# Kernel tuning notes

Hardware: AMD Instinct MI355X
Metric: run time of the kernel (lower is better)

## Reference

```python
import jax, jax.numpy as jnp
import numpy as np

B, NG, H, G, T0, T1 = 4096, 3000, 6, 30, 500, 50  # batch, genes, hidden, genes/term, leaf terms, mid terms
EPS = 1e-5  # BatchNorm1d default eps


def _bn(x, gamma, beta):
    # training-mode BatchNorm1d: biased batch stats over the batch axis
    m = x.mean(axis=0)
    v = ((x - m) ** 2).mean(axis=0)
    return gamma * (x - m) / jnp.sqrt(v + EPS) + beta


def setup_inputs() -> dict:
    key = jax.random.key(0)
    ks = iter(jax.random.split(key, 32))
    rn = lambda shape, s=0.05: jax.random.normal(next(ks), shape, dtype=jnp.float32) * s
    return dict(
        cell_features=jax.random.normal(next(ks), (B, NG), dtype=jnp.float32),
        Wdg=rn((T0 + T1 + 1, G, NG)), bdg=rn((T0 + T1 + 1, G)),
        W0=rn((T0, H, G)), b0=rn((T0, H)), gam0=jnp.ones((T0, H), jnp.float32), bet0=jnp.zeros((T0, H), jnp.float32),
        aw0=rn((T0, H)), ab0=rn((T0,)), av0=rn((T0,)), ac0=rn((T0,)),
        W1=rn((T1, H, 10 * H + G)), b1=rn((T1, H)), gam1=jnp.ones((T1, H), jnp.float32), bet1=jnp.zeros((T1, H), jnp.float32),
        aw1=rn((T1, H)), ab1=rn((T1,)), av1=rn((T1,)), ac1=rn((T1,)),
        W2=rn((H, T1 * H + G)), b2=rn((H,)), gam2=jnp.ones((H,), jnp.float32), bet2=jnp.zeros((H,), jnp.float32),
        aw2=rn((H,)), ab2=rn(()), av2=rn(()), ac2=rn(()),
    )


def reference(cell_features, Wdg, bdg,
              W0, b0, gam0, bet0, aw0, ab0, av0, ac0,
              W1, b1, gam1, bet1, aw1, ab1, av1, ac1,
              W2, b2, gam2, bet2, aw2, ab2, av2, ac2):
    # direct_gene_layer for every term: Linear(ngene -> genes_per_term), no activation
    dg = jnp.einsum('bn,tgn->btg', cell_features, Wdg) + bdg  # [B, 551, G]
    # ---- layer 0 (leaves): input = direct gene output only ----
    z0 = jnp.tanh(jnp.einsum('btg,thg->bth', dg[:, :T0], W0) + b0)
    n0 = _bn(z0, gam0, bet0)                                   # [B, T0, H]
    aux0 = jnp.tanh(jnp.einsum('bth,th->bt', n0, aw0) + ab0) * av0 + ac0
    # ---- layer 1: term t's children are leaves [10t, 10t+10); concat children + direct genes ----
    in1 = jnp.concatenate([n0.reshape(B, T1, 10 * H), dg[:, T0:T0 + T1]], axis=-1)  # [B, T1, 90]
    z1 = jnp.tanh(jnp.einsum('bti,thi->bth', in1, W1) + b1)
    n1 = _bn(z1, gam1, bet1)                                   # [B, T1, H]
    aux1 = jnp.tanh(jnp.einsum('bth,th->bt', n1, aw1) + ab1) * av1 + ac1
    # ---- root: children = all mid terms + direct genes ----
    in2 = jnp.concatenate([n1.reshape(B, T1 * H), dg[:, -1]], axis=-1)  # [B, 330]
    z2 = jnp.tanh(in2 @ W2.T + b2)
    n2 = _bn(z2, gam2, bet2)                                   # [B, H]
    aux2 = jnp.tanh(n2 @ aw2 + ab2) * av2 + ac2                # [B]
    # flatten (aux_out_map, term_NN_out_map) into one array for a single comparable output
    aux_all = jnp.concatenate([aux0, aux1, aux2[:, None]], axis=1)              # [B, 551]
    nn_all = jnp.concatenate([n0.reshape(B, -1), n1.reshape(B, -1), n2], axis=1)  # [B, 551*H]
    return jnp.concatenate([aux_all, nn_all], axis=1)          # [B, 3857]
```

## Files before the change

### kernel.cpp

```cpp
#include <hip/hip_runtime.h>
#include <hip/hip_bf16.h>

#define BATCH 4096
#define NGENE 3000
#define HID   6
#define GPT   30
#define T0N   500
#define T1N   50
#define KP    3008
#define MROWS 4608
#define OUTW  3857
#define BNEPS 1e-5f
#define NKT   47
#define BUFU  16384

typedef __attribute__((ext_vector_type(8))) __bf16 bf16x8;
typedef __attribute__((ext_vector_type(4))) float f32x4;
typedef __attribute__((ext_vector_type(8))) unsigned short ushort8;

__device__ __forceinline__ unsigned short f2bf(float f) {
  unsigned int u = __builtin_bit_cast(unsigned int, f);
  u = (u + 0x7fffu + ((u >> 16) & 1u)) >> 16;
  return (unsigned short)u;
}

__device__ __forceinline__ void gload_lds16(const void* g, void* l) {
  __builtin_amdgcn_global_load_lds(
      (const __attribute__((address_space(1))) unsigned int*)g,
      (__attribute__((address_space(3))) unsigned int*)l, 16, 0, 0);
}

__global__ void prep(const float* __restrict__ cell, const float* __restrict__ Wdg,
                     const float* __restrict__ bdg, const float* __restrict__ W0,
                     const float* __restrict__ b0,
                     ushort8* __restrict__ cellb, ushort8* __restrict__ abuf8,
                     float* __restrict__ bias) {
  int blk = blockIdx.x;
  if (blk < 6016) {
    int idx = blk * 256 + threadIdx.x;
    int r = idx / 376, c8 = idx - r * 376;
    int c = c8 * 8;
    ushort8 o = (ushort8)0;
    if (c < NGENE) {
      const float4* p = (const float4*)(cell + (size_t)r * NGENE + c);
      float4 a = p[0], b = p[1];
      o[0] = f2bf(a.x); o[1] = f2bf(a.y); o[2] = f2bf(a.z); o[3] = f2bf(a.w);
      o[4] = f2bf(b.x); o[5] = f2bf(b.y); o[6] = f2bf(b.z); o[7] = f2bf(b.w);
    }
    cellb[idx] = o;
  } else if (blk < 8378) {
    int idx = (blk - 6016) * 256 + threadIdx.x;
    if (idx >= 1608 * 376) return;
    int r = idx / 376, c8 = idx - r * 376;
    int c = c8 * 8;
    ushort8 o = (ushort8)0;
    if (r < 1530 && c < NGENE) {
      const float4* p = (const float4*)(Wdg + (size_t)(15000 + r) * NGENE + c);
      float4 a = p[0], b = p[1];
      o[0] = f2bf(a.x); o[1] = f2bf(a.y); o[2] = f2bf(a.z); o[3] = f2bf(a.w);
      o[4] = f2bf(b.x); o[5] = f2bf(b.y); o[6] = f2bf(b.z); o[7] = f2bf(b.w);
    }
    abuf8[(size_t)(3000 + r) * 376 + c8] = o;
  } else {
    int idx = (blk - 8378) * 256 + threadIdx.x;
    if (idx >= MROWS) return;
    float v = 0.f;
    if (idx < 3000) {
      int t = idx / HID;
      float s = b0[idx];
#pragma unroll
      for (int g = 0; g < GPT; ++g) s += W0[idx * GPT + g] * bdg[t * GPT + g];
      v = s;
    } else if (idx < 4530) {
      v = bdg[15000 + idx - 3000];
    }
    bias[idx] = v;
  }
}

__global__ void v0_build(const float* __restrict__ Wdg, const float* __restrict__ W0,
                         unsigned short* __restrict__ abuf) {
  int n = blockIdx.x * 256 + threadIdx.x;
  int t = blockIdx.y;
  if (n >= KP) return;
  bool valid = n < NGENE;
  float x[GPT];
#pragma unroll
  for (int g = 0; g < GPT; ++g)
    x[g] = valid ? Wdg[((size_t)(t * GPT + g)) * NGENE + n] : 0.f;
#pragma unroll
  for (int h = 0; h < HID; ++h) {
    const float* w = W0 + (t * HID + h) * GPT;
    float s = 0.f;
#pragma unroll
    for (int g = 0; g < GPT; ++g) s += x[g] * w[g];
    abuf[((size_t)(t * HID + h)) * KP + n] = valid ? f2bf(s) : (unsigned short)0;
  }
}

__global__ __launch_bounds__(256, 2) void gemm_fused(
    const unsigned short* __restrict__ A,
    const unsigned short* __restrict__ Bt,
    const float* __restrict__ bias,
    float* __restrict__ C,
    float* __restrict__ st) {
  extern __shared__ unsigned short smem[];
  const int tid  = threadIdx.x;
  const int wave = tid >> 6, lane = tid & 63;
  const int wm = wave >> 1, wn = wave & 1;
  const int quad = lane >> 4, fr = lane & 15;

  const int bid = blockIdx.x;
  const int wg  = (bid & 7) * 144 + (bid >> 3);
  const int m0 = (wg >> 5) * 128;
  const int n0 = (wg & 31) * 128;

  const unsigned short* srcA[4];
  const unsigned short* srcB[4];
#pragma unroll
  for (int i = 0; i < 4; ++i) {
    int c = i * 256 + tid;
    int row = c >> 3, sl = c & 7;
    srcA[i] = A  + (size_t)(m0 + row) * KP + ((sl ^ (row & 7)) << 3);
    srcB[i] = Bt + (size_t)(n0 + row) * KP + ((sl ^ (row & 7)) << 3);
  }

  f32x4 acc[4][4] = {};

#define STAGE(kt, buf)                                                        \
  {                                                                           \
    unsigned short* bb = smem + (buf) * BUFU;                                 \
    const int ko = (kt) * 64;                                                 \
    _Pragma("unroll")                                                         \
    for (int i = 0; i < 4; ++i) {                                             \
      gload_lds16(srcA[i] + ko, bb + i * 2048 + wave * 512);                  \
      gload_lds16(srcB[i] + ko, bb + 8192 + i * 2048 + wave * 512);           \
    }                                                                         \
  }

  STAGE(0, 0);
  STAGE(1, 1);
  asm volatile("s_waitcnt vmcnt(8)" ::: "memory");
  __builtin_amdgcn_s_barrier();

  const int ks0 = (quad ^ (fr & 7)) << 3;
  const int arow = (wm * 64 + fr) * 64;
  const int brow = 8192 + (wn * 64 + fr) * 64;

  int cur = 0;
  for (int t = 0; t < NKT; ++t) {
    const unsigned short* Ab = smem + cur * BUFU;
    bf16x8 af[4][2], bf[4][2];
#pragma unroll
    for (int tm = 0; tm < 4; ++tm) {
      af[tm][0] = *(const bf16x8*)(Ab + arow + tm * 1024 + ks0);
      af[tm][1] = *(const bf16x8*)(Ab + arow + tm * 1024 + (ks0 ^ 32));
    }
#pragma unroll
    for (int tn = 0; tn < 4; ++tn) {
      bf[tn][0] = *(const bf16x8*)(Ab + brow + tn * 1024 + ks0);
      bf[tn][1] = *(const bf16x8*)(Ab + brow + tn * 1024 + (ks0 ^ 32));
    }
    asm volatile("s_waitcnt lgkmcnt(0)" ::: "memory");
    __builtin_amdgcn_s_barrier();
    if (t + 2 < NKT) STAGE(t + 2, cur);
    __builtin_amdgcn_s_setprio(1);
#pragma unroll
    for (int s = 0; s < 2; ++s)
#pragma unroll
      for (int i = 0; i < 4; ++i)
#pragma unroll
        for (int j = 0; j < 4; ++j)
          acc[i][j] = __builtin_amdgcn_mfma_f32_16x16x32_bf16(af[i][s], bf[j][s], acc[i][j], 0, 0, 0);
    __builtin_amdgcn_s_setprio(0);
    if (t + 2 < NKT)      asm volatile("s_waitcnt vmcnt(8)" ::: "memory");
    else if (t + 1 < NKT) asm volatile("s_waitcnt vmcnt(0)" ::: "memory");
    __builtin_amdgcn_s_barrier();
    cur ^= 1;
  }
#undef STAGE

  const int mbase = m0 + wm * 64 + quad * 4;
  const int nbase = n0 + wn * 64 + fr;
#pragma unroll
  for (int i = 0; i < 4; ++i) {
#pragma unroll
    for (int rr = 0; rr < 4; ++rr) {
      const int m = mbase + i * 16 + rr;
      const float bia = bias[m];
      const bool act = m < 3000;
      float s = 0.f, q = 0.f;
#pragma unroll
      for (int j = 0; j < 4; ++j) {
        float v = acc[i][j][rr] + bia;
        if (act) v = tanhf(v);
        C[(size_t)m * BATCH + nbase + j * 16] = v;
        s += v; q += v * v;
      }
      if (act) {
#pragma unroll
        for (int off = 1; off < 16; off <<= 1) {
          s += __shfl_xor(s, off);
          q += __shfl_xor(q, off);
        }
        if (fr == 0) {
          atomicAdd(&st[2 * m], s);
          atomicAdd(&st[2 * m + 1], q);
        }
      }
    }
  }
}

__global__ void bnfin(const float* __restrict__ st, const float* __restrict__ gam,
                      const float* __restrict__ bet, float* __restrict__ ss, int ncols) {
  int c = blockIdx.x * 256 + threadIdx.x;
  if (c >= ncols) return;
  float m = st[2 * c] * (1.f / BATCH);
  float v = st[2 * c + 1] * (1.f / BATCH) - m * m;
  float sc = gam[c] * rsqrtf(v + BNEPS);
  ss[2 * c] = sc;
  ss[2 * c + 1] = bet[c] - m * sc;
}

__global__ void norm_emit_aux(const float* __restrict__ zT, const float* __restrict__ ss,
                              const float* __restrict__ aw, const float* __restrict__ ab,
                              const float* __restrict__ av, const float* __restrict__ ac,
                              float* __restrict__ out, int ncols, int outoff,
                              int auxoff, int nterm) {
  __shared__ float tile[66][65];
  int lane = threadIdx.x & 63, w = threadIdx.x >> 6;
  int c0 = blockIdx.x * 66, b0 = blockIdx.y * 64;
  for (int cc = w; cc < 66; cc += 4) {
    int c = c0 + cc;
    float n = 0.f;
    if (c < ncols)
      n = zT[(size_t)c * BATCH + b0 + lane] * ss[2 * c] + ss[2 * c + 1];
    tile[cc][lane] = n;
  }
  __syncthreads();
  for (int cl = lane; cl < 66; cl += 64) {
    int c = c0 + cl;
    if (c < ncols) {
#pragma unroll
      for (int i = 0; i < 16; ++i) {
        int rr = w * 16 + i;
        out[(size_t)(b0 + rr) * OUTW + outoff + c] = tile[cl][rr];
      }
    }
  }
  int t0 = c0 / 6;
  for (int tl = w; tl < 11; tl += 4) {
    int t = t0 + tl;
    if (t < nterm && c0 + tl * 6 < ncols) {
      float s = ab[t];
#pragma unroll
      for (int h = 0; h < HID; ++h) s += tile[tl * 6 + h][lane] * aw[t * HID + h];
      out[(size_t)(b0 + lane) * OUTW + auxoff + t] = tanhf(s) * av[t] + ac[t];
    }
  }
}

__global__ void layer1_zT(const float* __restrict__ C, const float* __restrict__ ss0,
                          const float* __restrict__ W1, const float* __restrict__ b1,
                          float* __restrict__ z1T, float* __restrict__ st) {
  int lane = threadIdx.x & 63, tg = threadIdx.x >> 6;
  int t = blockIdx.x * 4 + tg;
  if (t >= T1N) return;
  int b = blockIdx.y * 64 + lane;
  const float* z0T = C;
  const float* dgm = C + (size_t)3000 * BATCH;
  float x[90];
#pragma unroll
  for (int j = 0; j < 60; ++j) {
    int c = t * 60 + j;
    x[j] = z0T[(size_t)c * BATCH + b] * ss0[2 * c] + ss0[2 * c + 1];
  }
#pragma unroll
  for (int g = 0; g < GPT; ++g)
    x[60 + g] = dgm[(size_t)(t * GPT + g) * BATCH + b];
#pragma unroll
  for (int h = 0; h < HID; ++h) {
    int c = t * HID + h;
    const float* w = W1 + c * 90;
    float s = b1[c];
#pragma unroll
    for (int i = 0; i < 90; ++i) s += x[i] * w[i];
    float z = tanhf(s);
    z1T[(size_t)c * BATCH + b] = z;
    float s1 = z, s2 = z * z;
#pragma unroll
    for (int off = 32; off > 0; off >>= 1) {
      s1 += __shfl_down(s1, off);
      s2 += __shfl_down(s2, off);
    }
    if (lane == 0) {
      atomicAdd(&st[2 * c], s1);
      atomicAdd(&st[2 * c + 1], s2);
    }
  }
}

__global__ void root_zT(const float* __restrict__ C, const float* __restrict__ z1T,
                        const float* __restrict__ ss1, const float* __restrict__ W2,
                        const float* __restrict__ b2, float* __restrict__ z2T,
                        float* __restrict__ st) {
  int b = blockIdx.x * 256 + threadIdx.x;
  int lane = threadIdx.x & 63;
  const float* dgr = C + (size_t)4500 * BATCH;
  float s[HID];
#pragma unroll
  for (int h = 0; h < HID; ++h) s[h] = b2[h];
  for (int c = 0; c < 300; ++c) {
    float n = z1T[(size_t)c * BATCH + b] * ss1[2 * c] + ss1[2 * c + 1];
#pragma unroll
    for (int h = 0; h < HID; ++h) s[h] += n * W2[h * 330 + c];
  }
#pragma unroll
  for (int g = 0; g < GPT; ++g) {
    float d = dgr[(size_t)g * BATCH + b];
#pragma unroll
    for (int h = 0; h < HID; ++h) s[h] += d * W2[h * 330 + 300 + g];
  }
#pragma unroll
  for (int h = 0; h < HID; ++h) {
    float z = tanhf(s[h]);
    z2T[(size_t)h * BATCH + b] = z;
    float s1 = z, s2 = z * z;
#pragma unroll
    for (int off = 32; off > 0; off >>= 1) {
      s1 += __shfl_down(s1, off);
      s2 += __shfl_down(s2, off);
    }
    if (lane == 0) {
      atomicAdd(&st[2 * h], s1);
      atomicAdd(&st[2 * h + 1], s2);
    }
  }
}

__global__ void root_emit(const float* __restrict__ z2T, const float* __restrict__ ss2,
                          const float* __restrict__ aw2, const float* __restrict__ ab2,
                          const float* __restrict__ av2, const float* __restrict__ ac2,
                          float* __restrict__ out) {
  int b = blockIdx.x * 256 + threadIdx.x;
  float s = ab2[0];
#pragma unroll
  for (int h = 0; h < HID; ++h) {
    float n = z2T[(size_t)h * BATCH + b] * ss2[2 * h] + ss2[2 * h + 1];
    out[(size_t)b * OUTW + 3851 + h] = n;
    s += n * aw2[h];
  }
  out[(size_t)b * OUTW + 550] = tanhf(s) * av2[0] + ac2[0];
}

extern "C" void kernel_launch(void* const* d_in, const int* in_sizes, int n_in,
                              void* d_out, int out_size, void* d_ws, size_t ws_size,
                              hipStream_t stream) {
  (void)in_sizes; (void)n_in; (void)out_size; (void)ws_size;
  const float* cell = (const float*)d_in[0];
  const float* Wdg  = (const float*)d_in[1];
  const float* bdg  = (const float*)d_in[2];
  const float* W0   = (const float*)d_in[3];
  const float* b0   = (const float*)d_in[4];
  const float* gam0 = (const float*)d_in[5];
  const float* bet0 = (const float*)d_in[6];
  const float* aw0  = (const float*)d_in[7];
  const float* ab0  = (const float*)d_in[8];
  const float* av0  = (const float*)d_in[9];
  const float* ac0  = (const float*)d_in[10];
  const float* W1   = (const float*)d_in[11];
  const float* b1   = (const float*)d_in[12];
  const float* gam1 = (const float*)d_in[13];
  const float* bet1 = (const float*)d_in[14];
  const float* aw1  = (const float*)d_in[15];
  const float* ab1  = (const float*)d_in[16];
  const float* av1  = (const float*)d_in[17];
  const float* ac1  = (const float*)d_in[18];
  const float* W2   = (const float*)d_in[19];
  const float* b2   = (const float*)d_in[20];
  const float* gam2 = (const float*)d_in[21];
  const float* bet2 = (const float*)d_in[22];
  const float* aw2  = (const float*)d_in[23];
  const float* ab2  = (const float*)d_in[24];
  const float* av2  = (const float*)d_in[25];
  const float* ac2  = (const float*)d_in[26];
  float* out = (float*)d_out;

  char* ws = (char*)d_ws;
  unsigned short* cellb = (unsigned short*)(ws);
  unsigned short* abuf  = (unsigned short*)(ws + 24641536);
  float*          C     = (float*)(ws + 52363264);
  float*          z1T   = (float*)(ws + 127860736);
  float*          z2T   = (float*)(ws + 132775936);
  float*          st    = (float*)(ws + 132874240);
  float*          ssb   = (float*)(ws + 132907008);
  float*          bias  = (float*)(ws + 132939776);
  float* st0 = st,  *st1 = st + 2 * 3000,  *st2 = st + 2 * 3300;
  float* ss0 = ssb, *ss1 = ssb + 2 * 3000, *ss2 = ssb + 2 * 3300;

  static int s_attr = 0;
  if (!s_attr) {
    hipFuncSetAttribute(reinterpret_cast<const void*>(gemm_fused),
                        hipFuncAttributeMaxDynamicSharedMemorySize, 65536);
    s_attr = 1;
  }

  hipMemsetAsync(st, 0, 32768, stream);
  prep<<<8396, 256, 0, stream>>>(cell, Wdg, bdg, W0, b0,
                                 (ushort8*)cellb, (ushort8*)abuf, bias);
  v0_build<<<dim3(12, T0N), 256, 0, stream>>>(Wdg, W0, abuf);

  gemm_fused<<<1152, 256, 65536, stream>>>(abuf, cellb, bias, C, st0);

  bnfin<<<12, 256, 0, stream>>>(st0, gam0, bet0, ss0, 3000);
  norm_emit_aux<<<dim3(46, 64), 256, 0, stream>>>(C, ss0, aw0, ab0, av0, ac0,
                                                  out, 3000, 551, 0, 500);

  layer1_zT<<<dim3(13, 64), 256, 0, stream>>>(C, ss0, W1, b1, z1T, st1);
  bnfin<<<2, 256, 0, stream>>>(st1, gam1, bet1, ss1, 300);
  norm_emit_aux<<<dim3(5, 64), 256, 0, stream>>>(z1T, ss1, aw1, ab1, av1, ac1,
                                                 out, 300, 3551, 500, 50);

  root_zT<<<16, 256, 0, stream>>>(C, z1T, ss1, W2, b2, z2T, st2);
  bnfin<<<1, 256, 0, stream>>>(st2, gam2, bet2, ss2, 6);
  root_emit<<<16, 256, 0, stream>>>(z2T, ss2, aw2, ab2, av2, ac2, out);
}
```

Before: 699.9 us.

## Fuse BN-finalize and post-GEMM layers into fewer kernels, split MFMA halves

The separate bnfin launches are folded into their consumers, which now compute scale and shift from the raw sums. Layer-0 normalize/emit/aux is merged with the layer-1 compute, and layer-1 emit is merged with the root compute in one launch. This cuts kernel launches and avoids re-reading C for the normalized layer-0 values. The GEMM drops its XCD-aware block swizzle for a plain 2D grid, and issues the first half of the MFMAs before the LDS barrier to overlap LDS reads with compute. The root path still runs in only 16 blocks inside fuse_l2, and the plain grid may lose L2 locality.

```diff
diff --git a/kernel.cpp b/kernel.cpp
--- a/kernel.cpp
+++ b/kernel.cpp
@@ -110,10 +110,8 @@
   const int wm = wave >> 1, wn = wave & 1;
   const int quad = lane >> 4, fr = lane & 15;
 
-  const int bid = blockIdx.x;
-  const int wg  = (bid & 7) * 144 + (bid >> 3);
-  const int m0 = (wg >> 5) * 128;
-  const int n0 = (wg & 31) * 128;
+  const int m0 = blockIdx.y * 128;
+  const int n0 = blockIdx.x * 128;
 
   const unsigned short* srcA[4];
   const unsigned short* srcB[4];
@@ -152,26 +150,29 @@
     const unsigned short* Ab = smem + cur * BUFU;
     bf16x8 af[4][2], bf[4][2];
 #pragma unroll
-    for (int tm = 0; tm < 4; ++tm) {
-      af[tm][0] = *(const bf16x8*)(Ab + arow + tm * 1024 + ks0);
-      af[tm][1] = *(const bf16x8*)(Ab + arow + tm * 1024 + (ks0 ^ 32));
-    }
-#pragma unroll
-    for (int tn = 0; tn < 4; ++tn) {
-      bf[tn][0] = *(const bf16x8*)(Ab + brow + tn * 1024 + ks0);
-      bf[tn][1] = *(const bf16x8*)(Ab + brow + tn * 1024 + (ks0 ^ 32));
-    }
+    for (int tm = 0; tm < 4; ++tm) af[tm][0] = *(const bf16x8*)(Ab + arow + tm * 1024 + ks0);
+#pragma unroll
+    for (int tn = 0; tn < 4; ++tn) bf[tn][0] = *(const bf16x8*)(Ab + brow + tn * 1024 + ks0);
+#pragma unroll
+    for (int tm = 0; tm < 4; ++tm) af[tm][1] = *(const bf16x8*)(Ab + arow + tm * 1024 + (ks0 ^ 32));
+#pragma unroll
+    for (int tn = 0; tn < 4; ++tn) bf[tn][1] = *(const bf16x8*)(Ab + brow + tn * 1024 + (ks0 ^ 32));
+    __builtin_amdgcn_s_setprio(1);
+#pragma unroll
+    for (int i = 0; i < 4; ++i)
+#pragma unroll
+      for (int j = 0; j < 4; ++j)
+        acc[i][j] = __builtin_amdgcn_mfma_f32_16x16x32_bf16(af[i][0], bf[j][0], acc[i][j], 0, 0, 0);
+    __builtin_amdgcn_s_setprio(0);
     asm volatile("s_waitcnt lgkmcnt(0)" ::: "memory");
     __builtin_amdgcn_s_barrier();
     if (t + 2 < NKT) STAGE(t + 2, cur);
     __builtin_amdgcn_s_setprio(1);
 #pragma unroll
-    for (int s = 0; s < 2; ++s)
-#pragma unroll
-      for (int i = 0; i < 4; ++i)
-#pragma unroll
-        for (int j = 0; j < 4; ++j)
-          acc[i][j] = __builtin_amdgcn_mfma_f32_16x16x32_bf16(af[i][s], bf[j][s], acc[i][j], 0, 0, 0);
+    for (int i = 0; i < 4; ++i)
+#pragma unroll
+      for (int j = 0; j < 4; ++j)
+        acc[i][j] = __builtin_amdgcn_mfma_f32_16x16x32_bf16(af[i][1], bf[j][1], acc[i][j], 0, 0, 0);
     __builtin_amdgcn_s_setprio(0);
     if (t + 2 < NKT)      asm volatile("s_waitcnt vmcnt(8)" ::: "memory");
     else if (t + 1 < NKT) asm volatile("s_waitcnt vmcnt(0)" ::: "memory");
@@ -212,134 +213,155 @@
   }
 }
 
-__global__ void bnfin(const float* __restrict__ st, const float* __restrict__ gam,
-                      const float* __restrict__ bet, float* __restrict__ ss, int ncols) {
-  int c = blockIdx.x * 256 + threadIdx.x;
-  if (c >= ncols) return;
-  float m = st[2 * c] * (1.f / BATCH);
-  float v = st[2 * c + 1] * (1.f / BATCH) - m * m;
-  float sc = gam[c] * rsqrtf(v + BNEPS);
-  ss[2 * c] = sc;
-  ss[2 * c + 1] = bet[c] - m * sc;
-}
-
-__global__ void norm_emit_aux(const float* __restrict__ zT, const float* __restrict__ ss,
-                              const float* __restrict__ aw, const float* __restrict__ ab,
-                              const float* __restrict__ av, const float* __restrict__ ac,
-                              float* __restrict__ out, int ncols, int outoff,
-                              int auxoff, int nterm) {
-  __shared__ float tile[66][65];
-  int lane = threadIdx.x & 63, w = threadIdx.x >> 6;
-  int c0 = blockIdx.x * 66, b0 = blockIdx.y * 64;
-  for (int cc = w; cc < 66; cc += 4) {
-    int c = c0 + cc;
-    float n = 0.f;
-    if (c < ncols)
-      n = zT[(size_t)c * BATCH + b0 + lane] * ss[2 * c] + ss[2 * c + 1];
-    tile[cc][lane] = n;
+__global__ void fuse_l1(const float* __restrict__ C, const float* __restrict__ st0,
+                        const float* __restrict__ gam0, const float* __restrict__ bet0,
+                        const float* __restrict__ aw0, const float* __restrict__ ab0,
+                        const float* __restrict__ av0, const float* __restrict__ ac0,
+                        const float* __restrict__ W1, const float* __restrict__ b1,
+                        float* __restrict__ out, float* __restrict__ z1T,
+                        float* __restrict__ st1) {
+  __shared__ float tile[60][65];
+  __shared__ float dgt[30][65];
+  __shared__ float ssl[120];
+  const int t = blockIdx.x, b0 = blockIdx.y * 64;
+  const int lane = threadIdx.x & 63, w = threadIdx.x >> 6;
+  if (threadIdx.x < 60) {
+    int c = t * 60 + threadIdx.x;
+    float m = st0[2 * c] * (1.f / BATCH);
+    float v = st0[2 * c + 1] * (1.f / BATCH) - m * m;
+    float sc = gam0[c] * rsqrtf(v + BNEPS);
+    ssl[2 * threadIdx.x] = sc;
+    ssl[2 * threadIdx.x + 1] = bet0[c] - m * sc;
   }
   __syncthreads();
-  for (int cl = lane; cl < 66; cl += 64) {
-    int c = c0 + cl;
-    if (c < ncols) {
-#pragma unroll
-      for (int i = 0; i < 16; ++i) {
-        int rr = w * 16 + i;
-        out[(size_t)(b0 + rr) * OUTW + outoff + c] = tile[cl][rr];
-      }
-    }
-  }
-  int t0 = c0 / 6;
-  for (int tl = w; tl < 11; tl += 4) {
-    int t = t0 + tl;
-    if (t < nterm && c0 + tl * 6 < ncols) {
-      float s = ab[t];
-#pragma unroll
-      for (int h = 0; h < HID; ++h) s += tile[tl * 6 + h][lane] * aw[t * HID + h];
-      out[(size_t)(b0 + lane) * OUTW + auxoff + t] = tanhf(s) * av[t] + ac[t];
-    }
-  }
-}
-
-__global__ void layer1_zT(const float* __restrict__ C, const float* __restrict__ ss0,
-                          const float* __restrict__ W1, const float* __restrict__ b1,
-                          float* __restrict__ z1T, float* __restrict__ st) {
-  int lane = threadIdx.x & 63, tg = threadIdx.x >> 6;
-  int t = blockIdx.x * 4 + tg;
-  if (t >= T1N) return;
-  int b = blockIdx.y * 64 + lane;
-  const float* z0T = C;
-  const float* dgm = C + (size_t)3000 * BATCH;
-  float x[90];
-#pragma unroll
-  for (int j = 0; j < 60; ++j) {
-    int c = t * 60 + j;
-    x[j] = z0T[(size_t)c * BATCH + b] * ss0[2 * c] + ss0[2 * c + 1];
-  }
-#pragma unroll
-  for (int g = 0; g < GPT; ++g)
-    x[60 + g] = dgm[(size_t)(t * GPT + g) * BATCH + b];
-#pragma unroll
-  for (int h = 0; h < HID; ++h) {
-    int c = t * HID + h;
-    const float* w = W1 + c * 90;
-    float s = b1[c];
-#pragma unroll
-    for (int i = 0; i < 90; ++i) s += x[i] * w[i];
-    float z = tanhf(s);
-    z1T[(size_t)c * BATCH + b] = z;
-    float s1 = z, s2 = z * z;
-#pragma unroll
-    for (int off = 32; off > 0; off >>= 1) {
-      s1 += __shfl_down(s1, off);
-      s2 += __shfl_down(s2, off);
-    }
-    if (lane == 0) {
-      atomicAdd(&st[2 * c], s1);
-      atomicAdd(&st[2 * c + 1], s2);
-    }
-  }
-}
-
-__global__ void root_zT(const float* __restrict__ C, const float* __restrict__ z1T,
-                        const float* __restrict__ ss1, const float* __restrict__ W2,
-                        const float* __restrict__ b2, float* __restrict__ z2T,
-                        float* __restrict__ st) {
-  int b = blockIdx.x * 256 + threadIdx.x;
-  int lane = threadIdx.x & 63;
-  const float* dgr = C + (size_t)4500 * BATCH;
-  float s[HID];
-#pragma unroll
-  for (int h = 0; h < HID; ++h) s[h] = b2[h];
-  for (int c = 0; c < 300; ++c) {
-    float n = z1T[(size_t)c * BATCH + b] * ss1[2 * c] + ss1[2 * c + 1];
-#pragma unroll
-    for (int h = 0; h < HID; ++h) s[h] += n * W2[h * 330 + c];
-  }
-#pragma unroll
-  for (int g = 0; g < GPT; ++g) {
-    float d = dgr[(size_t)g * BATCH + b];
-#pragma unroll
-    for (int h = 0; h < HID; ++h) s[h] += d * W2[h * 330 + 300 + g];
-  }
-#pragma unroll
-  for (int h = 0; h < HID; ++h) {
-    float z = tanhf(s[h]);
-    z2T[(size_t)h * BATCH + b] = z;
-    float s1 = z, s2 = z * z;
-#pragma unroll
-    for (int off = 32; off > 0; off >>= 1) {
-      s1 += __shfl_down(s1, off);
-      s2 += __shfl_down(s2, off);
-    }
-    if (lane == 0) {
-      atomicAdd(&st[2 * h], s1);
-      atomicAdd(&st[2 * h + 1], s2);
-    }
-  }
-}
-
-__global__ void root_emit(const float* __restrict__ z2T, const float* __restrict__ ss2,
+  for (int cc = w; cc < 60; cc += 4)
+    tile[cc][lane] = C[(size_t)(t * 60 + cc) * BATCH + b0 + lane] * ssl[2 * cc] + ssl[2 * cc + 1];
+  for (int g = w; g < GPT; g += 4)
+    dgt[g][lane] = C[(size_t)(3000 + t * GPT + g) * BATCH + b0 + lane];
+  __syncthreads();
+  if (lane < 60) {
+#pragma unroll
+    for (int i = 0; i < 16; ++i)
+      out[(size_t)(b0 + w * 16 + i) * OUTW + 551 + t * 60 + lane] = tile[lane][w * 16 + i];
+  }
+  for (int tl = w; tl < 10; tl += 4) {
+    int tt = t * 10 + tl;
+    float s = ab0[tt];
+#pragma unroll
+    for (int h = 0; h < HID; ++h) s += tile[tl * 6 + h][lane] * aw0[tt * HID + h];
+    out[(size_t)(b0 + lane) * OUTW + tt] = tanhf(s) * av0[tt] + ac0[tt];
+  }
+  if (w < 3) {
+#pragma unroll
+    for (int hh = 0; hh < 2; ++hh) {
+      int h = w * 2 + hh, c = t * HID + h;
+      const float* wr = W1 + c * 90;
+      float s = b1[c];
+#pragma unroll
+      for (int j = 0; j < 60; ++j) s += tile[j][lane] * wr[j];
+#pragma unroll
+      for (int g = 0; g < GPT; ++g) s += dgt[g][lane] * wr[60 + g];
+      float z = tanhf(s);
+      z1T[(size_t)c * BATCH + b0 + lane] = z;
+      float s1 = z, s2 = z * z;
+#pragma unroll
+      for (int off = 32; off > 0; off >>= 1) {
+        s1 += __shfl_down(s1, off);
+        s2 += __shfl_down(s2, off);
+      }
+      if (lane == 0) {
+        atomicAdd(&st1[2 * c], s1);
+        atomicAdd(&st1[2 * c + 1], s2);
+      }
+    }
+  }
+}
+
+__global__ void fuse_l2(const float* __restrict__ C, const float* __restrict__ z1T,
+                        const float* __restrict__ st1,
+                        const float* __restrict__ gam1, const float* __restrict__ bet1,
+                        const float* __restrict__ aw1, const float* __restrict__ ab1,
+                        const float* __restrict__ av1, const float* __restrict__ ac1,
+                        const float* __restrict__ W2, const float* __restrict__ b2,
+                        float* __restrict__ out, float* __restrict__ z2T,
+                        float* __restrict__ st2) {
+  const int blk = blockIdx.x;
+  if (blk < 320) {
+    __shared__ float tile[60][65];
+    __shared__ float ssl[120];
+    const int q = blk >> 6, b0 = (blk & 63) * 64;
+    const int lane = threadIdx.x & 63, w = threadIdx.x >> 6;
+    if (threadIdx.x < 60) {
+      int c = q * 60 + threadIdx.x;
+      float m = st1[2 * c] * (1.f / BATCH);
+      float v = st1[2 * c + 1] * (1.f / BATCH) - m * m;
+      float sc = gam1[c] * rsqrtf(v + BNEPS);
+      ssl[2 * threadIdx.x] = sc;
+      ssl[2 * threadIdx.x + 1] = bet1[c] - m * sc;
+    }
+    __syncthreads();
+    for (int cc = w; cc < 60; cc += 4)
+      tile[cc][lane] = z1T[(size_t)(q * 60 + cc) * BATCH + b0 + lane] * ssl[2 * cc] + ssl[2 * cc + 1];
+    __syncthreads();
+    if (lane < 60) {
+#pragma unroll
+      for (int i = 0; i < 16; ++i)
+        out[(size_t)(b0 + w * 16 + i) * OUTW + 3551 + q * 60 + lane] = tile[lane][w * 16 + i];
+    }
+    for (int tl = w; tl < 10; tl += 4) {
+      int tt = q * 10 + tl;
+      float s = ab1[tt];
+#pragma unroll
+      for (int h = 0; h < HID; ++h) s += tile[tl * 6 + h][lane] * aw1[tt * HID + h];
+      out[(size_t)(b0 + lane) * OUTW + 500 + tt] = tanhf(s) * av1[tt] + ac1[tt];
+    }
+  } else {
+    __shared__ float ssl[600];
+    const int b = (blk - 320) * 256 + threadIdx.x;
+    const int lane = threadIdx.x & 63;
+    for (int c = threadIdx.x; c < 300; c += 256) {
+      float m = st1[2 * c] * (1.f / BATCH);
+      float v = st1[2 * c + 1] * (1.f / BATCH) - m * m;
+      float sc = gam1[c] * rsqrtf(v + BNEPS);
+      ssl[2 * c] = sc;
+      ssl[2 * c + 1] = bet1[c] - m * sc;
+    }
+    __syncthreads();
+    const float* dgr = C + (size_t)4500 * BATCH;
+    float s[HID];
+#pragma unroll
+    for (int h = 0; h < HID; ++h) s[h] = b2[h];
+    for (int c = 0; c < 300; ++c) {
+      float n = z1T[(size_t)c * BATCH + b] * ssl[2 * c] + ssl[2 * c + 1];
+#pragma unroll
+      for (int h = 0; h < HID; ++h) s[h] += n * W2[h * 330 + c];
+    }
+#pragma unroll
+    for (int g = 0; g < GPT; ++g) {
+      float d = dgr[(size_t)g * BATCH + b];
+#pragma unroll
+      for (int h = 0; h < HID; ++h) s[h] += d * W2[h * 330 + 300 + g];
+    }
+#pragma unroll
+    for (int h = 0; h < HID; ++h) {
+      float z = tanhf(s[h]);
+      z2T[(size_t)h * BATCH + b] = z;
+      float s1 = z, s2 = z * z;
+#pragma unroll
+      for (int off = 32; off > 0; off >>= 1) {
+        s1 += __shfl_down(s1, off);
+        s2 += __shfl_down(s2, off);
+      }
+      if (lane == 0) {
+        atomicAdd(&st2[2 * h], s1);
+        atomicAdd(&st2[2 * h + 1], s2);
+      }
+    }
+  }
+}
+
+__global__ void root_emit(const float* __restrict__ z2T, const float* __restrict__ st2,
+                          const float* __restrict__ gam2, const float* __restrict__ bet2,
                           const float* __restrict__ aw2, const float* __restrict__ ab2,
                           const float* __restrict__ av2, const float* __restrict__ ac2,
                           float* __restrict__ out) {
@@ -347,7 +369,11 @@
   float s = ab2[0];
 #pragma unroll
   for (int h = 0; h < HID; ++h) {
-    float n = z2T[(size_t)h * BATCH + b] * ss2[2 * h] + ss2[2 * h + 1];
+    float m = st2[2 * h] * (1.f / BATCH);
+    float v = st2[2 * h + 1] * (1.f / BATCH) - m * m;
+    float sc = gam2[h] * rsqrtf(v + BNEPS);
+    float sh = bet2[h] - m * sc;
+    float n = z2T[(size_t)h * BATCH + b] * sc + sh;
     out[(size_t)b * OUTW + 3851 + h] = n;
     s += n * aw2[h];
   }
@@ -394,10 +420,8 @@
   float*          z1T   = (float*)(ws + 127860736);
   float*          z2T   = (float*)(ws + 132775936);
   float*          st    = (float*)(ws + 132874240);
-  float*          ssb   = (float*)(ws + 132907008);
   float*          bias  = (float*)(ws + 132939776);
-  float* st0 = st,  *st1 = st + 2 * 3000,  *st2 = st + 2 * 3300;
-  float* ss0 = ssb, *ss1 = ssb + 2 * 3000, *ss2 = ssb + 2 * 3300;
+  float* st0 = st, *st1 = st + 2 * 3000, *st2 = st + 2 * 3300;
 
   static int s_attr = 0;
   if (!s_attr) {
@@ -411,18 +435,11 @@
                                  (ushort8*)cellb, (ushort8*)abuf, bias);
   v0_build<<<dim3(12, T0N), 256, 0, stream>>>(Wdg, W0, abuf);
 
-  gemm_fused<<<1152, 256, 65536, stream>>>(abuf, cellb, bias, C, st0);
-
-  bnfin<<<12, 256, 0, stream>>>(st0, gam0, bet0, ss0, 3000);
-  norm_emit_aux<<<dim3(46, 64), 256, 0, stream>>>(C, ss0, aw0, ab0, av0, ac0,
-                                                  out, 3000, 551, 0, 500);
-
-  layer1_zT<<<dim3(13, 64), 256, 0, stream>>>(C, ss0, W1, b1, z1T, st1);
-  bnfin<<<2, 256, 0, stream>>>(st1, gam1, bet1, ss1, 300);
-  norm_emit_aux<<<dim3(5, 64), 256, 0, stream>>>(z1T, ss1, aw1, ab1, av1, ac1,
-                                                 out, 300, 3551, 500, 50);
-
-  root_zT<<<16, 256, 0, stream>>>(C, z1T, ss1, W2, b2, z2T, st2);
-  bnfin<<<1, 256, 0, stream>>>(st2, gam2, bet2, ss2, 6);
-  root_emit<<<16, 256, 0, stream>>>(z2T, ss2, aw2, ab2, av2, ac2, out);
-}
+  gemm_fused<<<dim3(32, 36), 256, 65536, stream>>>(abuf, cellb, bias, C, st0);
+
+  fuse_l1<<<dim3(50, 64), 256, 0, stream>>>(C, st0, gam0, bet0, aw0, ab0, av0, ac0,
+                                            W1, b1, out, z1T, st1);
+  fuse_l2<<<336, 256, 0, stream>>>(C, z1T, st1, gam1, bet1, aw1, ab1, av1, ac1,
+                                   W2, b2, out, z2T, st2);
+  root_emit<<<16, 256, 0, stream>>>(z2T, st2, gam2, bet2, aw2, ab2, av2, ac2, out);
+}
```

New measurement: 626.9 us. -10.4%, faster.
